# Kernel tuning notes

Measured on AMD Instinct MI355X. Metric: run time of the kernel, lower is better.

## Reference

```python
import jax, jax.numpy as jnp
import numpy as np

EPS = 1e-6
LAM = 0.005


def setup_inputs() -> dict:
    key = jax.random.key(0)
    k1, k2, k3 = jax.random.split(key, 3)
    B, D, H, W, M = 16, 256, 128, 128, 4096
    z = jax.random.normal(k1, (B, D, H, W), dtype=jnp.float32)
    z_prime = jax.random.normal(k2, (B, D, H, W), dtype=jnp.float32)
    # Precomputed sampled pixel indices (flat over H*W). With randn inputs every
    # pixel passes the validity mask, so uniform sampling matches the original.
    flat_idx = jax.random.randint(k3, (B, M), 0, H * W, dtype=jnp.int32)
    return {"z": z, "z_prime": z_prime, "flat_idx": flat_idx}


def _gather_pixels(z, flat_idx):
    # z: (B, D, H, W), flat_idx: (B, M) -> (B*M, D)
    B, D, H, W = z.shape
    M = flat_idx.shape[1]
    z_flat = z.reshape(B, D, H * W)
    g = jnp.take_along_axis(z_flat, flat_idx[:, None, :], axis=2)  # (B, D, M)
    return g.transpose(0, 2, 1).reshape(B * M, D)


def _normalise(x):
    mean = jnp.mean(x, axis=0, keepdims=True)
    std = jnp.std(x, axis=0, keepdims=True, ddof=1)  # torch .std() is unbiased
    return (x - mean) / jnp.clip(std, EPS, None)


def reference(z, z_prime, flat_idx):
    D = z.shape[1]
    zm = _normalise(_gather_pixels(z, flat_idx))        # (N, D)
    zpm = _normalise(_gather_pixels(z_prime, flat_idx))  # (N, D)
    N = zm.shape[0]
    C = (zm.T @ zpm) / N                                 # (D, D)
    on_diag = jnp.diagonal(C)
    off_diag = C.reshape(-1)[1:].reshape(D - 1, D + 1)[:, :-1]
    loss = jnp.sum((1.0 - on_diag) ** 2) + LAM * jnp.sum(off_diag ** 2)
    return loss
```

## Files before the change

### kernel.cpp

```cpp
#include <hip/hip_runtime.h>
#include <hip/hip_bf16.h>

typedef short s16x8 __attribute__((ext_vector_type(8)));
typedef float f32x16 __attribute__((ext_vector_type(16)));

namespace {
constexpr int kB = 16;
constexpr int kD = 256;
constexpr int kHW = 16384;
constexpr int kM = 4096;
constexpr int kN = kB * kM;
constexpr int kWin = 1024;
constexpr int kNBlk = kB * (kHW / kWin);
constexpr int kKT = 16;
constexpr int kNIter = kWin / kKT;
constexpr float kLam = 0.005f;

__device__ __forceinline__ unsigned short f2bf(float f) {
    union { float f; unsigned u; } x{f};
    const unsigned r = x.u + 0x7FFFu + ((x.u >> 16) & 1u);
    return (unsigned short)(r >> 16);
}
}

#define BAR_SOFT()                                            \
    do {                                                      \
        asm volatile("s_waitcnt lgkmcnt(0)" ::: "memory");    \
        __builtin_amdgcn_s_barrier();                         \
    } while (0)

__global__ __launch_bounds__(256) void count_kernel(
    const int* __restrict__ flat_idx, int* __restrict__ cnt)
{
    __shared__ int h[kHW];
    const int t = threadIdx.x;
    const int b = blockIdx.x;
    for (int i = t; i < kHW; i += 256) h[i] = 0;
    __syncthreads();
    const int* bi = flat_idx + b * kM;
    for (int i = t; i < kM; i += 256) atomicAdd(&h[bi[i]], 1);
    __syncthreads();
    int* dst = cnt + b * kHW;
    for (int i = t; i < kHW; i += 256) dst[i] = h[i];
}

__global__ __launch_bounds__(512, 2) void fused_gram_kernel(
    const float* __restrict__ z, const float* __restrict__ zp,
    const int* __restrict__ cnt,
    float* __restrict__ partial, float* __restrict__ statsPart)
{
    __shared__ char smem[32768];

    const int bx = blockIdx.x;
    const int b = bx & (kB - 1);
    const int win0 = (bx >> 4) * kWin;
    const int t = threadIdx.x;
    const int w = t >> 6, lane = t & 63, l31 = lane & 31, half = lane >> 5;
    const int wr = w >> 2;
    const int wc = w & 3;
    const int rbase = t >> 2;
    const int cg = t & 3;

    const float* zb  = z  + (size_t)b * kD * kHW;
    const float* zpb = zp + (size_t)b * kD * kHW;
    const int* cb = cnt + b * kHW;

    f32x16 acc[4][2];
#pragma unroll
    for (int i = 0; i < 4; ++i)
#pragma unroll
        for (int j = 0; j < 2; ++j)
#pragma unroll
            for (int r = 0; r < 16; ++r) acc[i][j][r] = 0.f;

    float sA[2], ssA[2], sB[2], ssB[2];
#pragma unroll
    for (int q = 0; q < 2; ++q) { sA[q] = ssA[q] = sB[q] = ssB[q] = 0.f; }

    float4 va0[2], vb0[2], va1[2], vb1[2];
    int4 ci0, ci1;

#define LOAD_SET(S, kt)                                                     \
    {                                                                       \
        const int base_ = win0 + (kt) * kKT + cg * 4;                       \
        _Pragma("unroll")                                                   \
        for (int q = 0; q < 2; ++q) {                                       \
            const int row_ = rbase + 128 * q;                               \
            va##S[q] = *(const float4*)(zb  + (size_t)row_ * kHW + base_);  \
            vb##S[q] = *(const float4*)(zpb + (size_t)row_ * kHW + base_);  \
        }                                                                   \
        ci##S = *(const int4*)(cb + base_);                                 \
    }

#define CONV_SET(S, buf)                                                    \
    {                                                                       \
        char* As_ = smem + (buf) * 16384;                                   \
        char* Bs_ = As_ + 8192;                                             \
        const float cf_[4] = {(float)ci##S.x, (float)ci##S.y,               \
                              (float)ci##S.z, (float)ci##S.w};              \
        _Pragma("unroll")                                                   \
        for (int q = 0; q < 2; ++q) {                                       \
            const int row_ = rbase + 128 * q;                               \
            const float a_[4]  = {va##S[q].x, va##S[q].y, va##S[q].z, va##S[q].w}; \
            const float bb_[4] = {vb##S[q].x, vb##S[q].y, vb##S[q].z, vb##S[q].w}; \
            ushort4 pa_, pb_;                                               \
            unsigned short* pav_ = (unsigned short*)&pa_;                   \
            unsigned short* pbv_ = (unsigned short*)&pb_;                   \
            _Pragma("unroll")                                               \
            for (int j = 0; j < 4; ++j) {                                   \
                const float a2_ = a_[j] * a_[j];                            \
                const float b2_ = bb_[j] * bb_[j];                          \
                const float wb_ = cf_[j] * bb_[j];                          \
                sA[q] = fmaf(cf_[j], a_[j], sA[q]);                         \
                ssA[q] = fmaf(cf_[j], a2_, ssA[q]);                         \
                sB[q] = fmaf(cf_[j], bb_[j], sB[q]);                        \
                ssB[q] = fmaf(cf_[j], b2_, ssB[q]);                         \
                pav_[j] = f2bf(a_[j]);                                      \
                pbv_[j] = f2bf(wb_);                                        \
            }                                                               \
            const int off_ = (((cg >> 1) * 256 + row_) << 4) + ((cg & 1) << 3); \
            *(unsigned long long*)(As_ + off_) = *(unsigned long long*)&pa_; \
            *(unsigned long long*)(Bs_ + off_) = *(unsigned long long*)&pb_; \
        }                                                                   \
    }

    auto MFMA_STEP = [&](int buf) {
        const char* As = smem + buf * 16384;
        const char* Bs = As + 8192;
        s16x8 af[4], bfr[2];
#pragma unroll
        for (int rt = 0; rt < 4; ++rt) {
            const int row = 128 * wr + 32 * rt + l31;
            af[rt] = *(const s16x8*)(As + ((half * 256 + row) << 4));
        }
#pragma unroll
        for (int ct = 0; ct < 2; ++ct) {
            const int row = 64 * wc + 32 * ct + l31;
            bfr[ct] = *(const s16x8*)(Bs + ((half * 256 + row) << 4));
        }
#pragma unroll
        for (int rt = 0; rt < 4; ++rt)
#pragma unroll
            for (int ct = 0; ct < 2; ++ct)
                acc[rt][ct] = __builtin_amdgcn_mfma_f32_32x32x16_bf16(
                    af[rt], bfr[ct], acc[rt][ct], 0, 0, 0);
    };

    LOAD_SET(0, 0)
    CONV_SET(0, 0)
    LOAD_SET(1, 1)
    LOAD_SET(0, 2)
    BAR_SOFT();

    for (int kt = 0; kt < kNIter; kt += 2) {
        CONV_SET(1, 1)
        if (kt + 3 < kNIter) LOAD_SET(1, kt + 3)
        MFMA_STEP(0);
        BAR_SOFT();

        if (kt + 2 < kNIter) CONV_SET(0, 0)
        if (kt + 4 < kNIter) LOAD_SET(0, kt + 4)
        MFMA_STEP(1);
        BAR_SOFT();
    }
    __syncthreads();

    float* out = partial + (size_t)bx * (kD * kD);
#pragma unroll
    for (int rt = 0; rt < 4; ++rt)
#pragma unroll
        for (int ct = 0; ct < 2; ++ct)
#pragma unroll
            for (int r = 0; r < 16; ++r) {
                const int row = 128 * wr + 32 * rt + (r & 3) + 8 * (r >> 2) + 4 * half;
                const int col = 64 * wc + 32 * ct + l31;
                out[row * kD + col] = acc[rt][ct][r];
            }

    float* sd = (float*)smem;
#pragma unroll
    for (int q = 0; q < 2; ++q) {
        const int row = rbase + 128 * q;
        float* p = sd + (row * 4 + cg) * 4;
        p[0] = sA[q]; p[1] = ssA[q]; p[2] = sB[q]; p[3] = ssB[q];
    }
    __syncthreads();
    {
        const int row = t >> 1;
        const int pair = t & 1;
        float a0 = 0.f, a1 = 0.f;
#pragma unroll
        for (int g = 0; g < 4; ++g) {
            a0 += sd[(row * 4 + g) * 4 + 2 * pair];
            a1 += sd[(row * 4 + g) * 4 + 2 * pair + 1];
        }
        float* p = statsPart + ((size_t)bx * kD + row) * 4;
        p[2 * pair] = a0;
        p[2 * pair + 1] = a1;
    }
#undef LOAD_SET
#undef CONV_SET
}

__global__ __launch_bounds__(256) void reduce_gram_kernel(
    const float* __restrict__ partial, const float* __restrict__ statsPart,
    float* __restrict__ G, float* __restrict__ statsRed)
{
    const int d = blockIdx.x;
    const int e = threadIdx.x;
    float s = 0.f;
#pragma unroll 8
    for (int c = 0; c < kNBlk; ++c)
        s += partial[(size_t)c * (kD * kD) + d * kD + e];
    G[d * kD + e] = s;

    const float4 v = *(const float4*)(statsPart + ((size_t)e * kD + d) * 4);
    float x0 = v.x, x1 = v.y, x2 = v.z, x3 = v.w;
#pragma unroll
    for (int o = 32; o; o >>= 1) {
        x0 += __shfl_down(x0, o);
        x1 += __shfl_down(x1, o);
        x2 += __shfl_down(x2, o);
        x3 += __shfl_down(x3, o);
    }
    __shared__ float r[4][4];
    if ((e & 63) == 0) {
        r[e >> 6][0] = x0; r[e >> 6][1] = x1;
        r[e >> 6][2] = x2; r[e >> 6][3] = x3;
    }
    __syncthreads();
    if (e < 4) {
        statsRed[d * 4 + e] = r[0][e] + r[1][e] + r[2][e] + r[3][e];
    }
}

__global__ __launch_bounds__(256) void loss_kernel(
    const float* __restrict__ G, const float* __restrict__ statsRed,
    float* __restrict__ out)
{
    __shared__ float muA[kD], isA[kD], muB[kD], isB[kD];
    const int t = threadIdx.x;
    const float4 v = *(const float4*)(statsRed + t * 4);
    const float n = (float)kN;
    const float mA = v.x / n, mB = v.z / n;
    const float vA = (v.y - n * mA * mA) / (n - 1.f);
    const float vB = (v.w - n * mB * mB) / (n - 1.f);
    const float sdA = fmaxf(sqrtf(fmaxf(vA, 0.f)), 1e-6f);
    const float sdB = fmaxf(sqrtf(fmaxf(vB, 0.f)), 1e-6f);
    muA[t] = mA; isA[t] = 1.f / sdA;
    muB[t] = mB; isB[t] = 1.f / sdB;
    __syncthreads();

    float acc = 0.f;
    for (int d = 0; d < kD; ++d) {
        const int e = t;
        const float c = (G[d * kD + e] / n - muA[d] * muB[e]) * isA[d] * isB[e];
        if (d == e) { const float u = 1.f - c; acc += u * u; }
        else        { acc += kLam * c * c; }
    }
#pragma unroll
    for (int o = 32; o; o >>= 1) acc += __shfl_down(acc, o);
    __shared__ float r[4];
    if ((t & 63) == 0) r[t >> 6] = acc;
    __syncthreads();
    if (t == 0) out[0] = r[0] + r[1] + r[2] + r[3];
}

extern "C" void kernel_launch(void* const* d_in, const int* in_sizes, int n_in,
                              void* d_out, int out_size, void* d_ws, size_t ws_size,
                              hipStream_t stream) {
    const float* z  = (const float*)d_in[0];
    const float* zp = (const float*)d_in[1];
    const int* flat_idx = (const int*)d_in[2];
    float* out = (float*)d_out;

    char* ws = (char*)d_ws;
    int* cnt = (int*)ws;
    float* statsPart = (float*)(ws + (size_t)1 * 1024 * 1024);
    float* statsRed  = (float*)(ws + (size_t)2 * 1024 * 1024);
    float* G = (float*)(ws + (size_t)2 * 1024 * 1024 + 64 * 1024);
    float* partial = (float*)(ws + (size_t)16 * 1024 * 1024);

    count_kernel<<<kB, 256, 0, stream>>>(flat_idx, cnt);
    fused_gram_kernel<<<kNBlk, 512, 0, stream>>>(z, zp, cnt, partial, statsPart);
    reduce_gram_kernel<<<kD, 256, 0, stream>>>(partial, statsPart, G, statsRed);
    loss_kernel<<<1, 256, 0, stream>>>(G, statsRed, out);
}
```

Measured before the change: 207.1 us.

## Split Gram output columns across two blocks per window to double grid size

The fused Gram kernel now launches 512 blocks, each computing a 256x128 half of the per-window Gram tile instead of the full 256x256. Only the half-0 blocks accumulate z statistics, and each block loads only its half of z_prime rows. The per-block accumulator footprint shrinks, which allows four blocks per CU and gives more parallelism. The cost is that z is read twice from memory, and the reduce and stats kernels are adjusted to the new partial layout.

```diff
diff --git a/kernel.cpp b/kernel.cpp
--- a/kernel.cpp
+++ b/kernel.cpp
@@ -11,9 +11,9 @@
 constexpr int kM = 4096;
 constexpr int kN = kB * kM;
 constexpr int kWin = 1024;
-constexpr int kNBlk = kB * (kHW / kWin);
 constexpr int kKT = 16;
 constexpr int kNIter = kWin / kKT;
+constexpr int kNBlk = 512;
 constexpr float kLam = 0.005f;
 
 __device__ __forceinline__ unsigned short f2bf(float f) {
@@ -44,162 +44,169 @@
     for (int i = t; i < kHW; i += 256) dst[i] = h[i];
 }
 
-__global__ __launch_bounds__(512, 2) void fused_gram_kernel(
+__global__ __launch_bounds__(512, 4) void fused_gram_kernel(
     const float* __restrict__ z, const float* __restrict__ zp,
     const int* __restrict__ cnt,
     float* __restrict__ partial, float* __restrict__ statsPart)
 {
-    __shared__ char smem[32768];
+    __shared__ char smem[24576];
 
     const int bx = blockIdx.x;
     const int b = bx & (kB - 1);
-    const int win0 = (bx >> 4) * kWin;
+    const int win0 = ((bx >> 4) & 15) * kWin;
+    const int ch = bx >> 8;
     const int t = threadIdx.x;
     const int w = t >> 6, lane = t & 63, l31 = lane & 31, half = lane >> 5;
-    const int wr = w >> 2;
-    const int wc = w & 3;
-    const int rbase = t >> 2;
+    const int wr = w >> 1;
+    const int wc = w & 1;
+    const int row2 = t >> 2;
     const int cg = t & 3;
 
     const float* zb  = z  + (size_t)b * kD * kHW;
-    const float* zpb = zp + (size_t)b * kD * kHW;
+    const float* zpb = zp + ((size_t)b * kD + 128 * ch) * kHW;
     const int* cb = cnt + b * kHW;
 
-    f32x16 acc[4][2];
-#pragma unroll
-    for (int i = 0; i < 4; ++i)
+    f32x16 acc[2][2];
+#pragma unroll
+    for (int i = 0; i < 2; ++i)
 #pragma unroll
         for (int j = 0; j < 2; ++j)
 #pragma unroll
             for (int r = 0; r < 16; ++r) acc[i][j][r] = 0.f;
 
-    float sA[2], ssA[2], sB[2], ssB[2];
-#pragma unroll
-    for (int q = 0; q < 2; ++q) { sA[q] = ssA[q] = sB[q] = ssB[q] = 0.f; }
-
-    float4 va0[2], vb0[2], va1[2], vb1[2];
-    int4 ci0, ci1;
-
-#define LOAD_SET(S, kt)                                                     \
-    {                                                                       \
-        const int base_ = win0 + (kt) * kKT + cg * 4;                       \
-        _Pragma("unroll")                                                   \
-        for (int q = 0; q < 2; ++q) {                                       \
-            const int row_ = rbase + 128 * q;                               \
-            va##S[q] = *(const float4*)(zb  + (size_t)row_ * kHW + base_);  \
-            vb##S[q] = *(const float4*)(zpb + (size_t)row_ * kHW + base_);  \
-        }                                                                   \
-        ci##S = *(const int4*)(cb + base_);                                 \
-    }
-
-#define CONV_SET(S, buf)                                                    \
-    {                                                                       \
-        char* As_ = smem + (buf) * 16384;                                   \
-        char* Bs_ = As_ + 8192;                                             \
-        const float cf_[4] = {(float)ci##S.x, (float)ci##S.y,               \
-                              (float)ci##S.z, (float)ci##S.w};              \
-        _Pragma("unroll")                                                   \
-        for (int q = 0; q < 2; ++q) {                                       \
-            const int row_ = rbase + 128 * q;                               \
-            const float a_[4]  = {va##S[q].x, va##S[q].y, va##S[q].z, va##S[q].w}; \
-            const float bb_[4] = {vb##S[q].x, vb##S[q].y, vb##S[q].z, vb##S[q].w}; \
-            ushort4 pa_, pb_;                                               \
-            unsigned short* pav_ = (unsigned short*)&pa_;                   \
-            unsigned short* pbv_ = (unsigned short*)&pb_;                   \
-            _Pragma("unroll")                                               \
-            for (int j = 0; j < 4; ++j) {                                   \
-                const float a2_ = a_[j] * a_[j];                            \
-                const float b2_ = bb_[j] * bb_[j];                          \
-                const float wb_ = cf_[j] * bb_[j];                          \
-                sA[q] = fmaf(cf_[j], a_[j], sA[q]);                         \
-                ssA[q] = fmaf(cf_[j], a2_, ssA[q]);                         \
-                sB[q] = fmaf(cf_[j], bb_[j], sB[q]);                        \
-                ssB[q] = fmaf(cf_[j], b2_, ssB[q]);                         \
-                pav_[j] = f2bf(a_[j]);                                      \
-                pbv_[j] = f2bf(wb_);                                        \
-            }                                                               \
-            const int off_ = (((cg >> 1) * 256 + row_) << 4) + ((cg & 1) << 3); \
-            *(unsigned long long*)(As_ + off_) = *(unsigned long long*)&pa_; \
-            *(unsigned long long*)(Bs_ + off_) = *(unsigned long long*)&pb_; \
-        }                                                                   \
-    }
+    float sA[2], ssA[2], sB, ssB;
+    sA[0] = sA[1] = ssA[0] = ssA[1] = sB = ssB = 0.f;
+
+    float4 vA0, vA1, vB;
+    int4 ci;
+
+    auto LOAD = [&](int kt) {
+        const int base = win0 + kt * kKT + cg * 4;
+        vA0 = *(const float4*)(zb + (size_t)row2 * kHW + base);
+        vA1 = *(const float4*)(zb + (size_t)(row2 + 128) * kHW + base);
+        vB  = *(const float4*)(zpb + (size_t)row2 * kHW + base);
+        ci  = *(const int4*)(cb + base);
+    };
+
+    auto CONV = [&](int buf) {
+        char* As = smem + buf * 12288;
+        char* Bs = As + 8192;
+        const float cf[4] = {(float)ci.x, (float)ci.y, (float)ci.z, (float)ci.w};
+        const float4 va[2] = {vA0, vA1};
+#pragma unroll
+        for (int q = 0; q < 2; ++q) {
+            const int row = row2 + 128 * q;
+            const float a[4] = {va[q].x, va[q].y, va[q].z, va[q].w};
+            ushort4 pa;
+            unsigned short* pav = (unsigned short*)&pa;
+#pragma unroll
+            for (int j = 0; j < 4; ++j) {
+                if (ch == 0) {
+                    sA[q] = fmaf(cf[j], a[j], sA[q]);
+                    ssA[q] = fmaf(cf[j], a[j] * a[j], ssA[q]);
+                }
+                pav[j] = f2bf(a[j]);
+            }
+            const int off = (((cg >> 1) * 256 + row) << 4) + ((cg & 1) << 3);
+            *(unsigned long long*)(As + off) = *(unsigned long long*)&pa;
+        }
+        {
+            const float bb[4] = {vB.x, vB.y, vB.z, vB.w};
+            ushort4 pb;
+            unsigned short* pbv = (unsigned short*)&pb;
+#pragma unroll
+            for (int j = 0; j < 4; ++j) {
+                const float wb = cf[j] * bb[j];
+                sB = fmaf(cf[j], bb[j], sB);
+                ssB = fmaf(cf[j], bb[j] * bb[j], ssB);
+                pbv[j] = f2bf(wb);
+            }
+            const int off = (((cg >> 1) * 128 + row2) << 4) + ((cg & 1) << 3);
+            *(unsigned long long*)(Bs + off) = *(unsigned long long*)&pb;
+        }
+    };
 
     auto MFMA_STEP = [&](int buf) {
-        const char* As = smem + buf * 16384;
+        const char* As = smem + buf * 12288;
         const char* Bs = As + 8192;
-        s16x8 af[4], bfr[2];
-#pragma unroll
-        for (int rt = 0; rt < 4; ++rt) {
-            const int row = 128 * wr + 32 * rt + l31;
+        s16x8 af[2], bfr[2];
+#pragma unroll
+        for (int rt = 0; rt < 2; ++rt) {
+            const int row = 64 * wr + 32 * rt + l31;
             af[rt] = *(const s16x8*)(As + ((half * 256 + row) << 4));
         }
 #pragma unroll
         for (int ct = 0; ct < 2; ++ct) {
             const int row = 64 * wc + 32 * ct + l31;
-            bfr[ct] = *(const s16x8*)(Bs + ((half * 256 + row) << 4));
-        }
-#pragma unroll
-        for (int rt = 0; rt < 4; ++rt)
+            bfr[ct] = *(const s16x8*)(Bs + ((half * 128 + row) << 4));
+        }
+#pragma unroll
+        for (int rt = 0; rt < 2; ++rt)
 #pragma unroll
             for (int ct = 0; ct < 2; ++ct)
                 acc[rt][ct] = __builtin_amdgcn_mfma_f32_32x32x16_bf16(
                     af[rt], bfr[ct], acc[rt][ct], 0, 0, 0);
     };
 
-    LOAD_SET(0, 0)
-    CONV_SET(0, 0)
-    LOAD_SET(1, 1)
-    LOAD_SET(0, 2)
+    LOAD(0);
+    CONV(0);
+    LOAD(1);
     BAR_SOFT();
 
-    for (int kt = 0; kt < kNIter; kt += 2) {
-        CONV_SET(1, 1)
-        if (kt + 3 < kNIter) LOAD_SET(1, kt + 3)
-        MFMA_STEP(0);
+    for (int kt = 0; kt < kNIter; ++kt) {
+        if (kt + 1 < kNIter) CONV((kt + 1) & 1);
+        if (kt + 2 < kNIter) LOAD(kt + 2);
+        MFMA_STEP(kt & 1);
         BAR_SOFT();
-
-        if (kt + 2 < kNIter) CONV_SET(0, 0)
-        if (kt + 4 < kNIter) LOAD_SET(0, kt + 4)
-        MFMA_STEP(1);
-        BAR_SOFT();
-    }
-    __syncthreads();
-
-    float* out = partial + (size_t)bx * (kD * kD);
-#pragma unroll
-    for (int rt = 0; rt < 4; ++rt)
+    }
+    __syncthreads();
+
+    float* out = partial + (size_t)bx * (kD * 128);
+#pragma unroll
+    for (int rt = 0; rt < 2; ++rt)
 #pragma unroll
         for (int ct = 0; ct < 2; ++ct)
 #pragma unroll
             for (int r = 0; r < 16; ++r) {
-                const int row = 128 * wr + 32 * rt + (r & 3) + 8 * (r >> 2) + 4 * half;
+                const int row = 64 * wr + 32 * rt + (r & 3) + 8 * (r >> 2) + 4 * half;
                 const int col = 64 * wc + 32 * ct + l31;
-                out[row * kD + col] = acc[rt][ct][r];
-            }
-
-    float* sd = (float*)smem;
-#pragma unroll
-    for (int q = 0; q < 2; ++q) {
-        const int row = rbase + 128 * q;
-        float* p = sd + (row * 4 + cg) * 4;
-        p[0] = sA[q]; p[1] = ssA[q]; p[2] = sB[q]; p[3] = ssB[q];
-    }
-    __syncthreads();
-    {
-        const int row = t >> 1;
-        const int pair = t & 1;
-        float a0 = 0.f, a1 = 0.f;
-#pragma unroll
-        for (int g = 0; g < 4; ++g) {
-            a0 += sd[(row * 4 + g) * 4 + 2 * pair];
-            a1 += sd[(row * 4 + g) * 4 + 2 * pair + 1];
-        }
-        float* p = statsPart + ((size_t)bx * kD + row) * 4;
-        p[2 * pair] = a0;
-        p[2 * pair + 1] = a1;
-    }
-#undef LOAD_SET
-#undef CONV_SET
+                out[row * 128 + col] = acc[rt][ct][r];
+            }
+
+    float* sdA = (float*)smem;
+    float* sdB = (float*)(smem + 8192);
+    if (ch == 0) {
+#pragma unroll
+        for (int q = 0; q < 2; ++q) {
+            const int row = row2 + 128 * q;
+            sdA[(row * 4 + cg) * 2 + 0] = sA[q];
+            sdA[(row * 4 + cg) * 2 + 1] = ssA[q];
+        }
+    }
+    sdB[(row2 * 4 + cg) * 2 + 0] = sB;
+    sdB[(row2 * 4 + cg) * 2 + 1] = ssB;
+    __syncthreads();
+    if (t < kD) {
+        const int r = t;
+        float as_ = 0.f, ass_ = 0.f, bs_ = 0.f, bss_ = 0.f;
+        if (ch == 0) {
+#pragma unroll
+            for (int g = 0; g < 4; ++g) {
+                as_ += sdA[(r * 4 + g) * 2];
+                ass_ += sdA[(r * 4 + g) * 2 + 1];
+            }
+        }
+        if ((r >> 7) == ch) {
+            const int lb = r & 127;
+#pragma unroll
+            for (int g = 0; g < 4; ++g) {
+                bs_ += sdB[(lb * 4 + g) * 2];
+                bss_ += sdB[(lb * 4 + g) * 2 + 1];
+            }
+        }
+        float4 v = {as_, ass_, bs_, bss_};
+        *(float4*)(statsPart + ((size_t)bx * kD + r) * 4) = v;
+    }
 }
 
 __global__ __launch_bounds__(256) void reduce_gram_kernel(
@@ -208,14 +215,16 @@
 {
     const int d = blockIdx.x;
     const int e = threadIdx.x;
+    const int chh = e >> 7, el = e & 127;
     float s = 0.f;
 #pragma unroll 8
-    for (int c = 0; c < kNBlk; ++c)
-        s += partial[(size_t)c * (kD * kD) + d * kD + e];
+    for (int i = 0; i < 256; ++i)
+        s += partial[(size_t)(chh * 256 + i) * (kD * 128) + d * 128 + el];
     G[d * kD + e] = s;
 
-    const float4 v = *(const float4*)(statsPart + ((size_t)e * kD + d) * 4);
-    float x0 = v.x, x1 = v.y, x2 = v.z, x3 = v.w;
+    const float4 v1 = *(const float4*)(statsPart + ((size_t)e * kD + d) * 4);
+    const float4 v2 = *(const float4*)(statsPart + ((size_t)(e + 256) * kD + d) * 4);
+    float x0 = v1.x + v2.x, x1 = v1.y + v2.y, x2 = v1.z + v2.z, x3 = v1.w + v2.w;
 #pragma unroll
     for (int o = 32; o; o >>= 1) {
         x0 += __shfl_down(x0, o);
@@ -277,8 +286,8 @@
     char* ws = (char*)d_ws;
     int* cnt = (int*)ws;
     float* statsPart = (float*)(ws + (size_t)1 * 1024 * 1024);
-    float* statsRed  = (float*)(ws + (size_t)2 * 1024 * 1024);
-    float* G = (float*)(ws + (size_t)2 * 1024 * 1024 + 64 * 1024);
+    float* statsRed  = (float*)(ws + (size_t)3 * 1024 * 1024);
+    float* G = (float*)(ws + (size_t)3 * 1024 * 1024 + 64 * 1024);
     float* partial = (float*)(ws + (size_t)16 * 1024 * 1024);
 
     count_kernel<<<kB, 256, 0, stream>>>(flat_idx, cnt);
```

Result: slower. 223.5 us (+7.9%).
